# Performance work log

Measured on AMD Instinct MI355X. Metric: run time of the kernel, lower is better.

## Reference

```python
import jax, jax.numpy as jnp
import numpy as np


def log_g(x):
    # log of g(x) = where(x>=0, x+0.5, sigmoid(x))
    return jnp.where(x >= 0, jnp.log(jax.nn.relu(x) + 0.5), -jax.nn.softplus(-x))


def heinsen_scan_log(log_coeffs, log_values):
    # associative scan in log space over seq dim (axis=1)
    a_star = jnp.cumsum(log_coeffs, axis=1)
    log_h0_plus_b_star = jax.lax.cumlogsumexp(log_values - a_star, axis=1)
    return jnp.exp(a_star + log_h0_plus_b_star)


def setup_inputs() -> dict:
    key = jax.random.key(0)
    k1, k2, k3 = jax.random.split(key, 3)
    B, S, D_IN, D_INNER, D_OUT = 4, 4096, 1024, 1024, 1024
    x = jax.random.normal(k1, (B, S, D_IN), dtype=jnp.float32)
    # xavier_normal for Linear(d_in, 2*d_inner): std = sqrt(2/(fan_in+fan_out))
    std_hg = float(np.sqrt(2.0 / (D_IN + 2 * D_INNER)))
    W_hg = jax.random.normal(k2, (2 * D_INNER, D_IN), dtype=jnp.float32) * std_hg
    std_out = float(np.sqrt(2.0 / (D_INNER + D_OUT)))
    W_out = jax.random.normal(k3, (D_OUT, D_INNER), dtype=jnp.float32) * std_out
    return {"x": x, "W_hg": W_hg, "W_out": W_out}


def reference(x, W_hg, W_out):
    # x: [B,S,Din]; W_hg: [2*Dinner, Din]; W_out: [Dout, Dinner]
    hg = jnp.einsum("bsd,ed->bse", x, W_hg)
    hidden, gate = jnp.split(hg, 2, axis=-1)
    log_coeffs = -jax.nn.softplus(gate)        # log(1 - z)
    log_z = -jax.nn.softplus(-gate)            # log(z)
    log_values = log_z + log_g(hidden)
    h = heinsen_scan_log(log_coeffs, log_values)  # [B,S,Dinner]
    out = jnp.einsum("bsd,od->bso", h, W_out)
    return out
```

## Files before the change

kernel.cpp:

```cpp
#include <hip/hip_runtime.h>
#include <math.h>


typedef unsigned short ushort_t;
typedef __attribute__((ext_vector_type(4))) float f32x4;
typedef __attribute__((ext_vector_type(8))) __bf16 bf16x8;
typedef __attribute__((ext_vector_type(8))) unsigned short u16x8;

constexpr int Bsz  = 4;
constexpr int S    = 4096;
constexpr int Din  = 1024;
constexpr int Dh   = 1024;
constexpr int M    = Bsz * S;
constexpr int NCH  = 64;
constexpr int CL   = S / NCH;

__device__ __forceinline__ unsigned short f2bf(float f) {
    unsigned int u = __float_as_uint(f);
    unsigned int r = (u + 0x7fffu + ((u >> 16) & 1u)) >> 16;
    return (unsigned short)r;
}
__device__ __forceinline__ float bf2f(unsigned short u) {
    return __uint_as_float(((unsigned int)u) << 16);
}
__device__ __forceinline__ float sigf(float x) {
    x = fminf(fmaxf(x, -30.f), 30.f);
    return 1.0f / (1.0f + __expf(-x));
}
__device__ __forceinline__ void gld_lds16(const ushort_t* g, ushort_t* l) {
    __builtin_amdgcn_global_load_lds(
        (const __attribute__((address_space(1))) void*)g,
        (__attribute__((address_space(3))) void*)l, 16, 0, 0);
}

__global__ __launch_bounds__(256) void cvt_all(
    const float* __restrict__ x, const float* __restrict__ whg,
    const float* __restrict__ wout,
    ushort_t* __restrict__ xb, ushort_t* __restrict__ whgb,
    ushort_t* __restrict__ woutb)
{
    constexpr int NX = M * Din / 8;
    constexpr int NW = 2048 * 1024 / 8;
    const int i = blockIdx.x * 256 + threadIdx.x;
    const float* src; ushort_t* dst; int k;
    if (i < NX)            { src = x;    dst = xb;    k = i; }
    else if (i < NX + NW)  { src = whg;  dst = whgb;  k = i - NX; }
    else                   { src = wout; dst = woutb; k = i - NX - NW; }
    const float4 a = ((const float4*)src)[(size_t)k * 2];
    const float4 b = ((const float4*)src)[(size_t)k * 2 + 1];
    u16x8 o;
    o[0] = f2bf(a.x); o[1] = f2bf(a.y); o[2] = f2bf(a.z); o[3] = f2bf(a.w);
    o[4] = f2bf(b.x); o[5] = f2bf(b.y); o[6] = f2bf(b.z); o[7] = f2bf(b.w);
    ((u16x8*)dst)[k] = o;
}

template<bool OUT_BF16>
__global__ __launch_bounds__(512, 2) void gemm256(
    const ushort_t* __restrict__ A, int lda,
    const ushort_t* __restrict__ B, int ldb,
    void* __restrict__ Cout, int ldc, int K, int nbx_log2)
{
    __shared__ ushort_t lds[2][2][16384];
    char* const ldsb = (char*)&lds[0][0][0];

    const int NT = K >> 6;

    const int nwg = gridDim.x;
    const int cpx = nwg >> 3;
    const int bid = blockIdx.x;
    const int swz = (bid & 7) * cpx + (bid >> 3);
    const int bx  = swz & ((1 << nbx_log2) - 1);
    const int by  = swz >> nbx_log2;
    const int bm0 = by * 256;
    const int bn0 = bx * 256;

    const int t  = threadIdx.x;
    const int w  = t >> 6;
    const int l  = t & 63;
    const int wr = w >> 2;
    const int wc = w & 3;

    const int fr = l & 15;
    const int kg = l >> 4;
    const int a_row_byte = fr * 128;
    const int a_col0 = (kg * 16) ^ ((fr & 7) << 4);
    const int a_col1 = a_col0 ^ 64;
    const int b_row_byte = (wc * 64 + fr) * 64
                         + ((kg * 16) ^ (((fr >> 1) & 3) << 4));

    const int rA      = w * 16 + (l >> 3);
    const int rowA0p  = ((rA     ) >> 6) * 128 + ((rA     ) & 63);
    const int rowA1p  = ((rA +  8) >> 6) * 128 + ((rA +  8) & 63);
    const int acolA   = (((l & 7) * 16) ^ (((l >> 3) & 7) << 4)) >> 1;
    const ushort_t* aS0 = A + (size_t)(bm0 + rowA0p) * lda + acolA;
    const ushort_t* aS1 = A + (size_t)(bm0 + rowA1p) * lda + acolA;
    const size_t aMh = (size_t)64 * lda;
    const int brA  = w * 32 + (l >> 2);
    const int bcol = ((l & 3) ^ ((l >> 3) & 3)) * 8;
    const ushort_t* bS0 = B + (size_t)(bn0 + brA) * ldb + bcol;
    const ushort_t* bS1 = bS0 + (size_t)16 * ldb;

    auto stageA = [&](int Tt, int mh) {
        char* db = ldsb + (size_t)(Tt & 1) * 65536 + mh * 16384 + w * 2048;
        const size_t go = (size_t)mh * aMh + Tt * 64;
        gld_lds16(aS0 + go, (ushort_t*)db);
        gld_lds16(aS1 + go, (ushort_t*)(db + 1024));
    };
    auto stageB = [&](int Tt, int ks) {
        char* db = ldsb + (size_t)(Tt & 1) * 65536 + 32768 + ks * 16384 + w * 2048;
        const int go = Tt * 64 + ks * 32;
        gld_lds16(bS0 + go, (ushort_t*)db);
        gld_lds16(bS1 + go, (ushort_t*)(db + 1024));
    };

    f32x4 acc[8][4];
    #pragma unroll
    for (int i = 0; i < 8; ++i)
        #pragma unroll
        for (int j = 0; j < 4; ++j)
            acc[i][j] = (f32x4){0.f, 0.f, 0.f, 0.f};

    bf16x8 bfr0[4], bfr1[4];

    stageB(0, 0); stageB(0, 1); stageA(0, 0); stageA(0, 1);
    stageB(1, 0); stageB(1, 1); stageA(1, 0);
    asm volatile("s_waitcnt vmcnt(6)" ::: "memory");

    #pragma unroll 1
    for (int T = 0; T < NT; ++T) {
        if (T == NT - 1)
            asm volatile("s_waitcnt vmcnt(0)" ::: "memory");
        const char* abuf = ldsb + (size_t)(T & 1) * 65536;
        const char* bbuf = abuf + 32768;

        __builtin_amdgcn_s_barrier();
        __builtin_amdgcn_sched_barrier(0);
        if (T + 1 < NT) stageA(T + 1, 1);
        asm volatile("s_waitcnt vmcnt(8)" ::: "memory");
        __builtin_amdgcn_sched_barrier(0);
        {
            #pragma unroll
            for (int j = 0; j < 4; ++j)
                bfr0[j] = *(const bf16x8*)(bbuf + j * 1024 + b_row_byte);
            bf16x8 af[4];
            #pragma unroll
            for (int i = 0; i < 4; ++i)
                af[i] = *(const bf16x8*)(abuf + wr * 8192 + i * 2048 + a_row_byte + a_col0);
            __builtin_amdgcn_s_setprio(1);
            #pragma unroll
            for (int i = 0; i < 4; ++i)
                #pragma unroll
                for (int j = 0; j < 4; ++j)
                    acc[i][j] = __builtin_amdgcn_mfma_f32_16x16x32_bf16(
                        af[i], bfr0[j], acc[i][j], 0, 0, 0);
            __builtin_amdgcn_s_setprio(0);
            __builtin_amdgcn_sched_barrier(0);
        }

        __builtin_amdgcn_s_barrier();
        __builtin_amdgcn_sched_barrier(0);
        if (T + 2 < NT) stageB(T + 2, 0);
        asm volatile("s_waitcnt vmcnt(8)" ::: "memory");
        __builtin_amdgcn_sched_barrier(0);
        {
            #pragma unroll
            for (int j = 0; j < 4; ++j)
                bfr1[j] = *(const bf16x8*)(bbuf + 16384 + j * 1024 + b_row_byte);
            bf16x8 af[4];
            #pragma unroll
            for (int i = 0; i < 4; ++i)
                af[i] = *(const bf16x8*)(abuf + wr * 8192 + i * 2048 + a_row_byte + a_col1);
            __builtin_amdgcn_s_setprio(1);
            #pragma unroll
            for (int i = 0; i < 4; ++i)
                #pragma unroll
                for (int j = 0; j < 4; ++j)
                    acc[i][j] = __builtin_amdgcn_mfma_f32_16x16x32_bf16(
                        af[i], bfr1[j], acc[i][j], 0, 0, 0);
            __builtin_amdgcn_s_setprio(0);
            __builtin_amdgcn_sched_barrier(0);
        }

        __builtin_amdgcn_s_barrier();
        __builtin_amdgcn_sched_barrier(0);
        if (T + 2 < NT) stageB(T + 2, 1);
        asm volatile("s_waitcnt vmcnt(8)" ::: "memory");
        __builtin_amdgcn_sched_barrier(0);
        {
            bf16x8 af[4];
            #pragma unroll
            for (int i = 0; i < 4; ++i)
                af[i] = *(const bf16x8*)(abuf + 16384 + wr * 8192 + i * 2048 + a_row_byte + a_col0);
            __builtin_amdgcn_s_setprio(1);
            #pragma unroll
            for (int i = 0; i < 4; ++i)
                #pragma unroll
                for (int j = 0; j < 4; ++j)
                    acc[4 + i][j] = __builtin_amdgcn_mfma_f32_16x16x32_bf16(
                        af[i], bfr0[j], acc[4 + i][j], 0, 0, 0);
            __builtin_amdgcn_s_setprio(0);
            __builtin_amdgcn_sched_barrier(0);
        }

        __builtin_amdgcn_s_barrier();
        __builtin_amdgcn_sched_barrier(0);
        if (T + 2 < NT) stageA(T + 2, 0);
        asm volatile("s_waitcnt vmcnt(8)" ::: "memory");
        __builtin_amdgcn_sched_barrier(0);
        {
            bf16x8 af[4];
            #pragma unroll
            for (int i = 0; i < 4; ++i)
                af[i] = *(const bf16x8*)(abuf + 16384 + wr * 8192 + i * 2048 + a_row_byte + a_col1);
            __builtin_amdgcn_s_setprio(1);
            #pragma unroll
            for (int i = 0; i < 4; ++i)
                #pragma unroll
                for (int j = 0; j < 4; ++j)
                    acc[4 + i][j] = __builtin_amdgcn_mfma_f32_16x16x32_bf16(
                        af[i], bfr1[j], acc[4 + i][j], 0, 0, 0);
            __builtin_amdgcn_s_setprio(0);
            __builtin_amdgcn_sched_barrier(0);
        }
    }

    #pragma unroll
    for (int i = 0; i < 8; ++i) {
        #pragma unroll
        for (int j = 0; j < 4; ++j) {
            const int col = bn0 + wc * 64 + j * 16 + fr;
            #pragma unroll
            for (int r = 0; r < 4; ++r) {
                const int row = bm0 + wr * 128 + i * 16 + kg * 4 + r;
                if (OUT_BF16)
                    ((ushort_t*)Cout)[(size_t)row * ldc + col] = f2bf(acc[i][j][r]);
                else
                    ((float*)Cout)[(size_t)row * ldc + col] = acc[i][j][r];
            }
        }
    }
}


__global__ __launch_bounds__(256) void scan_stage1(
    const ushort_t* __restrict__ hg, float* __restrict__ Abuf,
    float* __restrict__ hlbuf)
{
    const int g     = blockIdx.x * 256 + threadIdx.x;
    const int d     = g & (Dh - 1);
    const int chunk = (g >> 10) & (NCH - 1);
    const int b     = g >> 16;
    const size_t rowbase = (size_t)(b * S + chunk * CL) * 2048;
    float h = 0.0f, Aacc = 1.0f;
    #pragma unroll 4
    for (int i = 0; i < CL; ++i) {
        const float hid  = bf2f(hg[rowbase + (size_t)i * 2048 + d]);
        const float gate = bf2f(hg[rowbase + (size_t)i * 2048 + 1024 + d]);
        const float z  = sigf(gate);
        const float c  = sigf(-gate);
        const float gv = (hid >= 0.0f) ? (hid + 0.5f) : sigf(hid);
        h = fmaf(c, h, z * gv);
        Aacc *= c;
    }
    const size_t o = (size_t)(b * NCH + chunk) * Dh + d;
    Abuf[o]  = Aacc;
    hlbuf[o] = h;
}

__global__ __launch_bounds__(256) void scan_stage2(
    const float* __restrict__ Abuf, const float* __restrict__ hlbuf,
    float* __restrict__ Hs)
{
    const int g = blockIdx.x * 256 + threadIdx.x;
    const int d = g & (Dh - 1);
    const int b = g >> 10;
    float h = 0.0f;
    for (int ch = 0; ch < NCH; ++ch) {
        const size_t o = (size_t)(b * NCH + ch) * Dh + d;
        Hs[o] = h;
        h = fmaf(Abuf[o], h, hlbuf[o]);
    }
}

__global__ __launch_bounds__(256) void scan_stage3(
    const ushort_t* __restrict__ hg, const float* __restrict__ Hs,
    ushort_t* __restrict__ hout)
{
    const int g     = blockIdx.x * 256 + threadIdx.x;
    const int d     = g & (Dh - 1);
    const int chunk = (g >> 10) & (NCH - 1);
    const int b     = g >> 16;
    const size_t rowbase = (size_t)(b * S + chunk * CL) * 2048;
    const size_t hbase   = (size_t)(b * S + chunk * CL) * 1024 + d;
    float h = Hs[(size_t)(b * NCH + chunk) * Dh + d];
    #pragma unroll 4
    for (int i = 0; i < CL; ++i) {
        const size_t ro = rowbase + (size_t)i * 2048;
        const float hid  = bf2f(hg[ro + d]);
        const float gate = bf2f(hg[ro + 1024 + d]);
        const float z  = sigf(gate);
        const float c  = sigf(-gate);
        const float gv = (hid >= 0.0f) ? (hid + 0.5f) : sigf(hid);
        h = fmaf(c, h, z * gv);
        hout[hbase + (size_t)i * 1024] = f2bf(h);
    }
}

extern "C" void kernel_launch(void* const* d_in, const int* in_sizes, int n_in,
                              void* d_out, int out_size, void* d_ws, size_t ws_size,
                              hipStream_t stream)
{
    (void)in_sizes; (void)n_in; (void)out_size; (void)ws_size;
    const float* x    = (const float*)d_in[0];
    const float* Whg  = (const float*)d_in[1];
    const float* Wout = (const float*)d_in[2];
    float* out = (float*)d_out;

    ushort_t* hgbuf = (ushort_t*)d_ws;
    ushort_t* xb    = hgbuf + (size_t)M * 2048;
    ushort_t* whgb  = xb + (size_t)M * 1024;
    ushort_t* woutb = whgb + (size_t)2048 * 1024;
    float*    Abuf  = (float*)(woutb + (size_t)1024 * 1024);
    float*    hlbuf = Abuf + (size_t)Bsz * NCH * Dh;
    float*    Hsbuf = hlbuf + (size_t)Bsz * NCH * Dh;

    const dim3 blk(256);

    cvt_all<<<dim3(9728), blk, 0, stream>>>(x, Whg, Wout, xb, whgb, woutb);

    gemm256<true><<<dim3(512), dim3(512), 0, stream>>>(
        xb, Din, whgb, Din, hgbuf, 2048, Din, 3);

    scan_stage1<<<dim3(Bsz * NCH * Dh / 256), blk, 0, stream>>>(hgbuf, Abuf, hlbuf);
    scan_stage2<<<dim3(Bsz * Dh / 256), blk, 0, stream>>>(Abuf, hlbuf, Hsbuf);
    scan_stage3<<<dim3(Bsz * NCH * Dh / 256), blk, 0, stream>>>(hgbuf, Hsbuf, xb);

    gemm256<false><<<dim3(256), dim3(512), 0, stream>>>(
        xb, Dh, woutb, Din, out, 1024, Dh, 2);
}
```

Before: 211.6 us.

## Restructure GEMM prefetch pipeline and stage fp32 epilogue through LDS

Reworks the double-buffered GEMM main loop to prefetch only one tile ahead. Each k-sub-step's global->LDS load is issued right after that step's LDS fragment reads, with one barrier per step, and the last iteration is peeled so no conditional waits remain in the loop. The fp32 output epilogue now transposes accumulators through LDS and writes 16-byte vectorized nontemporal stores instead of scalar 4-byte stores. The aim is to cut barrier and waitcnt overhead and improve store coalescing. The cost is a shallower prefetch depth, which may expose more global-memory latency.

```diff
diff --git a/kernel.cpp b/kernel.cpp
--- a/kernel.cpp
+++ b/kernel.cpp
@@ -122,22 +122,29 @@
 
     bf16x8 bfr0[4], bfr1[4];
 
-    stageB(0, 0); stageB(0, 1); stageA(0, 0); stageA(0, 1);
-    stageB(1, 0); stageB(1, 1); stageA(1, 0);
-    asm volatile("s_waitcnt vmcnt(6)" ::: "memory");
+    stageA(0, 0); stageB(0, 0); stageB(0, 1); stageA(0, 1);
+    asm volatile("s_waitcnt vmcnt(4)" ::: "memory");
+    __builtin_amdgcn_s_barrier();
+    __builtin_amdgcn_sched_barrier(0);
+
+    #define MFMA16(ACCB, AF, BF)                                          \
+        asm volatile("s_waitcnt lgkmcnt(0)" ::: "memory");                \
+        __builtin_amdgcn_sched_barrier(0);                                \
+        __builtin_amdgcn_s_setprio(1);                                    \
+        _Pragma("unroll")                                                 \
+        for (int i = 0; i < 4; ++i)                                       \
+            _Pragma("unroll")                                             \
+            for (int j = 0; j < 4; ++j)                                   \
+                acc[ACCB + i][j] = __builtin_amdgcn_mfma_f32_16x16x32_bf16( \
+                    AF[i], BF[j], acc[ACCB + i][j], 0, 0, 0);             \
+        __builtin_amdgcn_s_setprio(0);                                    \
+        __builtin_amdgcn_sched_barrier(0);
 
     #pragma unroll 1
-    for (int T = 0; T < NT; ++T) {
-        if (T == NT - 1)
-            asm volatile("s_waitcnt vmcnt(0)" ::: "memory");
+    for (int T = 0; T < NT - 1; ++T) {
         const char* abuf = ldsb + (size_t)(T & 1) * 65536;
         const char* bbuf = abuf + 32768;
 
-        __builtin_amdgcn_s_barrier();
-        __builtin_amdgcn_sched_barrier(0);
-        if (T + 1 < NT) stageA(T + 1, 1);
-        asm volatile("s_waitcnt vmcnt(8)" ::: "memory");
-        __builtin_amdgcn_sched_barrier(0);
         {
             #pragma unroll
             for (int j = 0; j < 4; ++j)
@@ -146,97 +153,145 @@
             #pragma unroll
             for (int i = 0; i < 4; ++i)
                 af[i] = *(const bf16x8*)(abuf + wr * 8192 + i * 2048 + a_row_byte + a_col0);
-            __builtin_amdgcn_s_setprio(1);
-            #pragma unroll
-            for (int i = 0; i < 4; ++i)
+            stageA(T + 1, 0);
+            __builtin_amdgcn_sched_barrier(0);
+            asm volatile("s_waitcnt vmcnt(4)" ::: "memory");
+            __builtin_amdgcn_s_barrier();
+            __builtin_amdgcn_sched_barrier(0);
+            MFMA16(0, af, bfr0)
+        }
+        {
+            #pragma unroll
+            for (int j = 0; j < 4; ++j)
+                bfr1[j] = *(const bf16x8*)(bbuf + 16384 + j * 1024 + b_row_byte);
+            bf16x8 af[4];
+            #pragma unroll
+            for (int i = 0; i < 4; ++i)
+                af[i] = *(const bf16x8*)(abuf + wr * 8192 + i * 2048 + a_row_byte + a_col1);
+            stageB(T + 1, 0);
+            __builtin_amdgcn_sched_barrier(0);
+            asm volatile("s_waitcnt vmcnt(4)" ::: "memory");
+            __builtin_amdgcn_s_barrier();
+            __builtin_amdgcn_sched_barrier(0);
+            MFMA16(0, af, bfr1)
+        }
+        {
+            bf16x8 af[4];
+            #pragma unroll
+            for (int i = 0; i < 4; ++i)
+                af[i] = *(const bf16x8*)(abuf + 16384 + wr * 8192 + i * 2048 + a_row_byte + a_col0);
+            stageB(T + 1, 1);
+            __builtin_amdgcn_sched_barrier(0);
+            __builtin_amdgcn_s_barrier();
+            __builtin_amdgcn_sched_barrier(0);
+            MFMA16(4, af, bfr0)
+        }
+        {
+            bf16x8 af[4];
+            #pragma unroll
+            for (int i = 0; i < 4; ++i)
+                af[i] = *(const bf16x8*)(abuf + 16384 + wr * 8192 + i * 2048 + a_row_byte + a_col1);
+            stageA(T + 1, 1);
+            __builtin_amdgcn_sched_barrier(0);
+            asm volatile("s_waitcnt vmcnt(4)" ::: "memory");
+            __builtin_amdgcn_s_barrier();
+            __builtin_amdgcn_sched_barrier(0);
+            MFMA16(4, af, bfr1)
+        }
+    }
+
+    {
+        const int T = NT - 1;
+        const char* abuf = ldsb + (size_t)(T & 1) * 65536;
+        const char* bbuf = abuf + 32768;
+        {
+            #pragma unroll
+            for (int j = 0; j < 4; ++j)
+                bfr0[j] = *(const bf16x8*)(bbuf + j * 1024 + b_row_byte);
+            bf16x8 af[4];
+            #pragma unroll
+            for (int i = 0; i < 4; ++i)
+                af[i] = *(const bf16x8*)(abuf + wr * 8192 + i * 2048 + a_row_byte + a_col0);
+            __builtin_amdgcn_sched_barrier(0);
+            asm volatile("s_waitcnt vmcnt(2)" ::: "memory");
+            __builtin_amdgcn_s_barrier();
+            __builtin_amdgcn_sched_barrier(0);
+            MFMA16(0, af, bfr0)
+        }
+        {
+            #pragma unroll
+            for (int j = 0; j < 4; ++j)
+                bfr1[j] = *(const bf16x8*)(bbuf + 16384 + j * 1024 + b_row_byte);
+            bf16x8 af[4];
+            #pragma unroll
+            for (int i = 0; i < 4; ++i)
+                af[i] = *(const bf16x8*)(abuf + wr * 8192 + i * 2048 + a_row_byte + a_col1);
+            __builtin_amdgcn_sched_barrier(0);
+            asm volatile("s_waitcnt vmcnt(0)" ::: "memory");
+            __builtin_amdgcn_s_barrier();
+            __builtin_amdgcn_sched_barrier(0);
+            MFMA16(0, af, bfr1)
+        }
+        {
+            bf16x8 af[4];
+            #pragma unroll
+            for (int i = 0; i < 4; ++i)
+                af[i] = *(const bf16x8*)(abuf + 16384 + wr * 8192 + i * 2048 + a_row_byte + a_col0);
+            __builtin_amdgcn_sched_barrier(0);
+            __builtin_amdgcn_s_barrier();
+            __builtin_amdgcn_sched_barrier(0);
+            MFMA16(4, af, bfr0)
+        }
+        {
+            bf16x8 af[4];
+            #pragma unroll
+            for (int i = 0; i < 4; ++i)
+                af[i] = *(const bf16x8*)(abuf + 16384 + wr * 8192 + i * 2048 + a_row_byte + a_col1);
+            __builtin_amdgcn_sched_barrier(0);
+            __builtin_amdgcn_s_barrier();
+            __builtin_amdgcn_sched_barrier(0);
+            MFMA16(4, af, bfr1)
+        }
+    }
+    #undef MFMA16
+
+    __builtin_amdgcn_s_barrier();
+
+    if (OUT_BF16) {
+        #pragma unroll
+        for (int i = 0; i < 8; ++i) {
+            #pragma unroll
+            for (int j = 0; j < 4; ++j) {
+                const int col = bn0 + wc * 64 + j * 16 + fr;
                 #pragma unroll
-                for (int j = 0; j < 4; ++j)
-                    acc[i][j] = __builtin_amdgcn_mfma_f32_16x16x32_bf16(
-                        af[i], bfr0[j], acc[i][j], 0, 0, 0);
-            __builtin_amdgcn_s_setprio(0);
-            __builtin_amdgcn_sched_barrier(0);
-        }
-
-        __builtin_amdgcn_s_barrier();
-        __builtin_amdgcn_sched_barrier(0);
-        if (T + 2 < NT) stageB(T + 2, 0);
-        asm volatile("s_waitcnt vmcnt(8)" ::: "memory");
-        __builtin_amdgcn_sched_barrier(0);
-        {
-            #pragma unroll
-            for (int j = 0; j < 4; ++j)
-                bfr1[j] = *(const bf16x8*)(bbuf + 16384 + j * 1024 + b_row_byte);
-            bf16x8 af[4];
-            #pragma unroll
-            for (int i = 0; i < 4; ++i)
-                af[i] = *(const bf16x8*)(abuf + wr * 8192 + i * 2048 + a_row_byte + a_col1);
-            __builtin_amdgcn_s_setprio(1);
-            #pragma unroll
-            for (int i = 0; i < 4; ++i)
+                for (int r = 0; r < 4; ++r) {
+                    const int row = bm0 + wr * 128 + i * 16 + kg * 4 + r;
+                    ((ushort_t*)Cout)[(size_t)row * ldc + col] = f2bf(acc[i][j][r]);
+                }
+            }
+        }
+    } else {
+        float* lw = (float*)(ldsb + w * 4352);
+        #pragma unroll 1
+        for (int i = 0; i < 8; ++i) {
+            #pragma unroll
+            for (int j = 0; j < 4; ++j)
                 #pragma unroll
-                for (int j = 0; j < 4; ++j)
-                    acc[i][j] = __builtin_amdgcn_mfma_f32_16x16x32_bf16(
-                        af[i], bfr1[j], acc[i][j], 0, 0, 0);
-            __builtin_amdgcn_s_setprio(0);
-            __builtin_amdgcn_sched_barrier(0);
-        }
-
-        __builtin_amdgcn_s_barrier();
-        __builtin_amdgcn_sched_barrier(0);
-        if (T + 2 < NT) stageB(T + 2, 1);
-        asm volatile("s_waitcnt vmcnt(8)" ::: "memory");
-        __builtin_amdgcn_sched_barrier(0);
-        {
-            bf16x8 af[4];
-            #pragma unroll
-            for (int i = 0; i < 4; ++i)
-                af[i] = *(const bf16x8*)(abuf + 16384 + wr * 8192 + i * 2048 + a_row_byte + a_col0);
-            __builtin_amdgcn_s_setprio(1);
-            #pragma unroll
-            for (int i = 0; i < 4; ++i)
-                #pragma unroll
-                for (int j = 0; j < 4; ++j)
-                    acc[4 + i][j] = __builtin_amdgcn_mfma_f32_16x16x32_bf16(
-                        af[i], bfr0[j], acc[4 + i][j], 0, 0, 0);
-            __builtin_amdgcn_s_setprio(0);
-            __builtin_amdgcn_sched_barrier(0);
-        }
-
-        __builtin_amdgcn_s_barrier();
-        __builtin_amdgcn_sched_barrier(0);
-        if (T + 2 < NT) stageA(T + 2, 0);
-        asm volatile("s_waitcnt vmcnt(8)" ::: "memory");
-        __builtin_amdgcn_sched_barrier(0);
-        {
-            bf16x8 af[4];
-            #pragma unroll
-            for (int i = 0; i < 4; ++i)
-                af[i] = *(const bf16x8*)(abuf + 16384 + wr * 8192 + i * 2048 + a_row_byte + a_col1);
-            __builtin_amdgcn_s_setprio(1);
-            #pragma unroll
-            for (int i = 0; i < 4; ++i)
-                #pragma unroll
-                for (int j = 0; j < 4; ++j)
-                    acc[4 + i][j] = __builtin_amdgcn_mfma_f32_16x16x32_bf16(
-                        af[i], bfr1[j], acc[4 + i][j], 0, 0, 0);
-            __builtin_amdgcn_s_setprio(0);
-            __builtin_amdgcn_sched_barrier(0);
-        }
-    }
-
-    #pragma unroll
-    for (int i = 0; i < 8; ++i) {
-        #pragma unroll
-        for (int j = 0; j < 4; ++j) {
-            const int col = bn0 + wc * 64 + j * 16 + fr;
-            #pragma unroll
-            for (int r = 0; r < 4; ++r) {
-                const int row = bm0 + wr * 128 + i * 16 + kg * 4 + r;
-                if (OUT_BF16)
-                    ((ushort_t*)Cout)[(size_t)row * ldc + col] = f2bf(acc[i][j][r]);
-                else
-                    ((float*)Cout)[(size_t)row * ldc + col] = acc[i][j][r];
+                for (int r = 0; r < 4; ++r)
+                    lw[(kg * 4 + r) * 68 + j * 16 + fr] = acc[i][j][r];
+            asm volatile("s_waitcnt lgkmcnt(0)" ::: "memory");
+            __builtin_amdgcn_sched_barrier(0);
+            #pragma unroll
+            for (int ci = 0; ci < 4; ++ci) {
+                const int rr = ci * 4 + kg;
+                const f32x4 v = *(const f32x4*)&lw[rr * 68 + (l & 15) * 4];
+                const int row = bm0 + wr * 128 + i * 16 + rr;
+                const int col = bn0 + wc * 64 + (l & 15) * 4;
+                __builtin_nontemporal_store(
+                    v, (f32x4*)((float*)Cout + (size_t)row * ldc + col));
             }
+            asm volatile("s_waitcnt lgkmcnt(0)" ::: "memory");
+            __builtin_amdgcn_sched_barrier(0);
         }
     }
 }
```

After: 241.1 us. 1.14x slower.
